# Kernel tuning notes

Measured on AMD Instinct MI355X. Metric: run time of the kernel, lower is better.

Reference implementation:

```python
import jax, jax.numpy as jnp
import numpy as np

B, T, N = 32, 24, 512
DIM_IN, DIM_OUT, HID, EMB = 64, 2, 128, 16
NEG_SLOPE = 0.01  # nn.LeakyReLU default


def leaky_relu(x):
    return jnp.where(x >= 0, x, NEG_SLOPE * x)


def setup_inputs() -> dict:
    key = jax.random.key(0)
    ks = jax.random.split(key, 11)
    return {
        "eb": jax.random.normal(ks[0], (B, T, N, DIM_IN), jnp.float32),
        "time_eb": jax.random.normal(ks[1], (B, T, EMB), jnp.float32),
        "node_eb": jax.random.normal(ks[2], (N, EMB), jnp.float32),
        # ln1: Linear(dim_in, hidden) stored as [dim_in, hidden] (x @ W + b)
        "W1": jax.random.normal(ks[3], (DIM_IN, HID), jnp.float32) / np.sqrt(DIM_IN),
        "b1": jax.random.normal(ks[4], (HID,), jnp.float32) * 0.01,
        # ln3: Linear(hidden, dim_out)
        "W3": jax.random.normal(ks[5], (HID, DIM_OUT), jnp.float32) / np.sqrt(HID),
        "b3": jax.random.normal(ks[6], (DIM_OUT,), jnp.float32) * 0.01,
        "weights_pool_spa": jax.random.normal(ks[7], (EMB, HID, HID), jnp.float32),
        "bias_pool_spa": jax.random.normal(ks[8], (EMB, HID), jnp.float32),
        "weights_pool_tem": jax.random.normal(ks[9], (EMB, HID, HID), jnp.float32),
        "bias_pool_tem": jax.random.normal(ks[10], (EMB, HID), jnp.float32),
    }


def reference(eb, time_eb, node_eb, W1, b1, W3, b3,
              weights_pool_spa, bias_pool_spa,
              weights_pool_tem, bias_pool_tem):
    # eb: [b,t,n,dim_in] -> [b,t,n,hidden]
    eb_out = eb @ W1 + b1
    # spatial hypernetwork: per-node weight [n,hid,hid] and bias [n,hid]
    weights_spa = jnp.einsum('nd,dio->nio', node_eb, weights_pool_spa)
    bias_spa = node_eb @ bias_pool_spa  # [n,hid]
    out_spa = leaky_relu(jnp.einsum('btni,nio->btno', eb_out, weights_spa) + bias_spa)
    # temporal hypernetwork: per-(b,t) weight [b,t,hid,hid] and bias [b,t,1,hid]
    weights_tem = jnp.einsum('btd,dio->btio', time_eb, weights_pool_tem)
    bias_tem = (time_eb @ bias_pool_tem)[:, :, None, :]
    out_tem = leaky_relu(jnp.einsum('btni,btio->btno', out_spa, weights_tem) + bias_tem)
    logits = out_tem @ W3 + b3  # [b,t,n,dim_out]
    return logits
```

## Files before the change

kernel.cpp:

```cpp
#include <hip/hip_runtime.h>
#include <hip/hip_bf16.h>
#include <stdint.h>

#define BT   768
#define NN   512
#define DIN  64
#define HID  128
#define EMB  16
#define SLOPE 0.01f

typedef __attribute__((ext_vector_type(8))) short bf16x8;
typedef __attribute__((ext_vector_type(4))) float f32x4;
typedef __attribute__((ext_vector_type(4))) short short4v;

__device__ __forceinline__ short f2bf(float f) {
    uint32_t u = __float_as_uint(f);
    u += 0x7fff + ((u >> 16) & 1);
    return (short)(u >> 16);
}
__device__ __forceinline__ float bf2f(short s) {
    return __uint_as_float(((uint32_t)(unsigned short)s) << 16);
}

static const size_t OFF_WCOMB = 0;
static const size_t OFF_WTEM  = 8388608;
static const size_t OFF_BSPA  = 33554432;
static const size_t OFF_BTEM  = 33816576;
static const size_t OFF_Q     = 34209792;
static const size_t OFF_PTT   = 34217984;
static const size_t OFF_PTS2  = 34742272;
static const size_t OFF_H2    = 35004416;

__global__ __launch_bounds__(256)
void k_prep(const float* __restrict__ pool_spa, const float* __restrict__ pool_tem,
            const float* __restrict__ W1, const float* __restrict__ b1,
            const float* __restrict__ bp_spa, const float* __restrict__ bp_tem,
            const float* __restrict__ node_eb, const float* __restrict__ time_eb,
            short* __restrict__ ptt, short* __restrict__ pts2,
            float* __restrict__ qtab, float* __restrict__ bspa,
            float* __restrict__ btem)
{
    const int b = blockIdx.x, t = threadIdx.x;
    __shared__ short smem[26112];

    if (b < 64) {
        const int d = b >> 2, o0 = (b & 3) * 32;
        short* s = smem;
        #pragma unroll
        for (int c = 0; c < 16; ++c) {
            int e = c * 256 + t;
            int i = e >> 5, oo = e & 31;
            s[oo * 136 + i] = f2bf(pool_tem[(d * HID + i) * HID + o0 + oo]);
        }
        __syncthreads();
        #pragma unroll
        for (int c = 0; c < 8; ++c) {
            int e = c * 256 + t;
            int oo = e >> 6, ii = (e & 63) * 2;
            uint32_t lo = (unsigned short)s[oo * 136 + ii];
            uint32_t hi = (unsigned short)s[oo * 136 + ii + 1];
            ((uint32_t*)ptt)[((d * HID + o0 + oo) * HID + ii) >> 1] = lo | (hi << 16);
        }
        return;
    }
    if (b < 224) {
        int q = (b - 64) * 256 + t;
        const float *bp, *emb; float* outp;
        if (q < NN * 32) { bp = bp_spa; emb = node_eb; outp = bspa; }
        else { q -= NN * 32; bp = bp_tem; emb = time_eb; outp = btem; }
        const int n = q >> 5, oq = q & 31;
        float4 a = make_float4(0.f, 0.f, 0.f, 0.f);
        #pragma unroll
        for (int d = 0; d < EMB; ++d) {
            float e = emb[n * EMB + d];
            float4 bv = ((const float4*)bp)[d * 32 + oq];
            a.x += e * bv.x; a.y += e * bv.y; a.z += e * bv.z; a.w += e * bv.w;
        }
        ((float4*)outp)[q] = a;
        return;
    }
    if (b < 226) {
        const int dbase = (b - 224) * 8;
        if (t < 128) {
            float a[8] = {};
            for (int i = 0; i < HID; ++i) {
                float bv = b1[i];
                #pragma unroll
                for (int dd = 0; dd < 8; ++dd)
                    a[dd] += bv * pool_spa[((dbase + dd) * HID + i) * HID + t];
            }
            #pragma unroll
            for (int dd = 0; dd < 8; ++dd) qtab[(dbase + dd) * HID + t] = a[dd];
        }
        return;
    }
    {
        const int d = b - 226;
        const int wave = t >> 6, lane = t & 63, quad = lane >> 4, l15 = lane & 15;
        const int m0 = wave * 32;
        short* sPT  = smem;
        short* sW1b = smem + 128 * 136;
        #pragma unroll
        for (int c = 0; c < 64; ++c) {
            int idx = c * 256 + t;
            int i = idx >> 7, o = idx & 127;
            sPT[o * 136 + i] = f2bf(pool_spa[(d * HID + i) * HID + o]);
        }
        #pragma unroll
        for (int c = 0; c < 32; ++c) {
            int idx = c * 256 + t;
            sW1b[(idx >> 7) * 136 + (idx & 127)] = f2bf(W1[idx]);
        }
        __syncthreads();
        f32x4 acc[2][4] = {};
        #pragma unroll
        for (int kc = 0; kc < 4; ++kc) {
            bf16x8 a0 = *(const bf16x8*)(sPT + (m0 + l15) * 136 + kc * 32 + quad * 8);
            bf16x8 a1 = *(const bf16x8*)(sPT + (m0 + 16 + l15) * 136 + kc * 32 + quad * 8);
            #pragma unroll
            for (int tc = 0; tc < 4; ++tc) {
                bf16x8 bb = *(const bf16x8*)(sW1b + (tc * 16 + l15) * 136 + kc * 32 + quad * 8);
                acc[0][tc] = __builtin_amdgcn_mfma_f32_16x16x32_bf16(a0, bb, acc[0][tc], 0, 0, 0);
                acc[1][tc] = __builtin_amdgcn_mfma_f32_16x16x32_bf16(a1, bb, acc[1][tc], 0, 0, 0);
            }
        }
        __syncthreads();
        short* sO = smem;
        #pragma unroll
        for (int tr = 0; tr < 2; ++tr)
            #pragma unroll
            for (int tc = 0; tc < 4; ++tc)
                #pragma unroll
                for (int r = 0; r < 4; ++r)
                    sO[(m0 + tr * 16 + quad * 4 + r) * 72 + tc * 16 + l15] = f2bf(acc[tr][tc][r]);
        __syncthreads();
        #pragma unroll
        for (int c = 0; c < 4; ++c) {
            int idx = c * 256 + t;
            int row = idx >> 3, ko = (idx & 7) * 8;
            *(bf16x8*)(pts2 + (size_t)d * 8192 + row * 64 + ko) =
                *(const bf16x8*)(sO + row * 72 + ko);
        }
    }
}

__global__ __launch_bounds__(256)
void k_genw(const short* __restrict__ pts2, const short* __restrict__ ptt,
            const float* __restrict__ node_eb, const float* __restrict__ time_eb,
            short* __restrict__ wcomb, short* __restrict__ wtem)
{
    const int t = threadIdx.x, b = blockIdx.x;
    int nb, cq, stride;
    const short* pool; const float* emb; short* outp;
    if (b < 64) {
        nb = b >> 3; cq = (b & 7) * 256 + t; stride = 2048;
        pool = pts2; emb = node_eb; outp = wcomb;
    } else {
        int bb = b - 64;
        nb = bb >> 4; cq = (bb & 15) * 256 + t; stride = 4096;
        pool = ptt; emb = time_eb; outp = wtem;
    }
    __shared__ float sEmb[64 * EMB];
    #pragma unroll
    for (int c = 0; c < 4; ++c) {
        int idx = c * 256 + t;
        sEmb[idx] = emb[nb * 64 * EMB + idx];
    }
    __syncthreads();
    float4 p[EMB];
    #pragma unroll
    for (int d = 0; d < EMB; ++d) {
        short4v v = ((const short4v*)pool)[d * stride + cq];
        p[d] = make_float4(bf2f(v.x), bf2f(v.y), bf2f(v.z), bf2f(v.w));
    }
    for (int nn = 0; nn < 64; ++nn) {
        float4 a = make_float4(0.f, 0.f, 0.f, 0.f);
        #pragma unroll
        for (int d = 0; d < EMB; ++d) {
            float e = sEmb[nn * EMB + d];
            a.x += e * p[d].x; a.y += e * p[d].y;
            a.z += e * p[d].z; a.w += e * p[d].w;
        }
        short4v o;
        o.x = f2bf(a.x); o.y = f2bf(a.y); o.z = f2bf(a.z); o.w = f2bf(a.w);
        ((short4v*)outp)[(size_t)(nb * 64 + nn) * stride + cq] = o;
    }
}

__global__ __launch_bounds__(256)
void k_spatial(const float* __restrict__ eb, const short* __restrict__ wcomb,
               const float* __restrict__ bspa, const float* __restrict__ qtab,
               const float* __restrict__ node_eb, short* __restrict__ h2)
{
    const int n = blockIdx.x, R0 = blockIdx.y * 64;
    const int t = threadIdx.x;
    const int wave = t >> 6, lane = t & 63, quad = lane >> 4, l15 = lane & 15;
    const int m0 = (wave >> 1) * 32, n0 = (wave & 1) * 64;

    __shared__ short smem[13824];
    short* sEb  = smem;
    short* sW   = smem + 64 * 72;
    short* sOut = smem;

    float4 ev[4];
    #pragma unroll
    for (int c = 0; c < 4; ++c) {
        int idx = c * 256 + t;
        int r = idx >> 4, kq = (idx & 15) * 4;
        ev[c] = *(const float4*)(eb + ((size_t)(R0 + r) * NN + n) * DIN + kq);
    }
    bf16x8 wreg[4];
    {
        const bf16x8* src = (const bf16x8*)(wcomb + (size_t)n * 8192);
        #pragma unroll
        for (int c = 0; c < 4; ++c) wreg[c] = src[c * 256 + t];
    }
    float bsr[4];
    #pragma unroll
    for (int tc = 0; tc < 4; ++tc) {
        int col = n0 + tc * 16 + l15;
        float a = bspa[n * HID + col];
        #pragma unroll
        for (int d = 0; d < EMB; ++d)
            a += node_eb[n * EMB + d] * qtab[d * HID + col];
        bsr[tc] = a;
    }
    #pragma unroll
    for (int c = 0; c < 4; ++c) {
        int idx = c * 256 + t;
        int r = idx >> 4, kq = (idx & 15) * 4;
        short4v s;
        s.x = f2bf(ev[c].x); s.y = f2bf(ev[c].y);
        s.z = f2bf(ev[c].z); s.w = f2bf(ev[c].w);
        *(short4v*)(sEb + r * 72 + kq) = s;
    }
    #pragma unroll
    for (int c = 0; c < 4; ++c) {
        int idx = c * 256 + t;
        *(bf16x8*)(sW + (idx >> 3) * 72 + (idx & 7) * 8) = wreg[c];
    }
    __syncthreads();

    f32x4 acc[2][4] = {};
    #pragma unroll
    for (int kc = 0; kc < 2; ++kc) {
        bf16x8 a0 = *(const bf16x8*)(sEb + (m0 + l15) * 72 + kc * 32 + quad * 8);
        bf16x8 a1 = *(const bf16x8*)(sEb + (m0 + 16 + l15) * 72 + kc * 32 + quad * 8);
        #pragma unroll
        for (int tc = 0; tc < 4; ++tc) {
            bf16x8 bfr = *(const bf16x8*)(sW + (n0 + tc * 16 + l15) * 72 + kc * 32 + quad * 8);
            acc[0][tc] = __builtin_amdgcn_mfma_f32_16x16x32_bf16(a0, bfr, acc[0][tc], 0, 0, 0);
            acc[1][tc] = __builtin_amdgcn_mfma_f32_16x16x32_bf16(a1, bfr, acc[1][tc], 0, 0, 0);
        }
    }
    __syncthreads();

    #pragma unroll
    for (int tr = 0; tr < 2; ++tr)
        #pragma unroll
        for (int tc = 0; tc < 4; ++tc) {
            int col = n0 + tc * 16 + l15;
            #pragma unroll
            for (int r = 0; r < 4; ++r) {
                float v = acc[tr][tc][r] + bsr[tc];
                v = (v >= 0.f) ? v : SLOPE * v;
                sOut[(m0 + tr * 16 + quad * 4 + r) * 136 + col] = f2bf(v);
            }
        }
    __syncthreads();
    #pragma unroll
    for (int c = 0; c < 4; ++c) {
        int idx = c * 256 + t;
        int row = idx >> 4, col = (idx & 15) * 8;
        *(bf16x8*)(h2 + ((size_t)(R0 + row) * NN + n) * HID + col) =
            *(const bf16x8*)(sOut + row * 136 + col);
    }
}

__global__ __launch_bounds__(256)
void k_temporal(const short* __restrict__ h2, const short* __restrict__ wtem,
                const float* __restrict__ btem, const float* __restrict__ W3,
                const float* __restrict__ b3, float* __restrict__ out)
{
    const int R = blockIdx.x, nbase = blockIdx.y * 256;
    const int t = threadIdx.x;
    const int wave = t >> 6, lane = t & 63, quad = lane >> 4, l15 = lane & 15;
    const int m0 = wave * 16;

    __shared__ short sWt[128 * 136];
    __shared__ short sH2[64 * 136];

    bf16x8 wv[8];
    {
        const bf16x8* src = (const bf16x8*)(wtem + (size_t)R * 16384);
        #pragma unroll
        for (int c = 0; c < 8; ++c) wv[c] = src[c * 256 + t];
    }
    bf16x8 hreg[4];
    {
        const bf16x8* src = (const bf16x8*)(h2 + ((size_t)R * NN + nbase) * HID);
        #pragma unroll
        for (int c = 0; c < 4; ++c) hreg[c] = src[c * 256 + t];
    }
    float btr[8], w3r0[8], w3r1[8];
    #pragma unroll
    for (int tc = 0; tc < 8; ++tc) {
        int o = tc * 16 + l15;
        btr[tc] = btem[R * HID + o];
        w3r0[tc] = W3[2 * o]; w3r1[tc] = W3[2 * o + 1];
    }
    const float b30 = b3[0], b31 = b3[1];

    #pragma unroll
    for (int c = 0; c < 8; ++c) {
        int idx = c * 256 + t;
        *(bf16x8*)(sWt + (idx >> 4) * 136 + (idx & 15) * 8) = wv[c];
    }
    #pragma unroll
    for (int c = 0; c < 4; ++c) {
        int idx = c * 256 + t;
        *(bf16x8*)(sH2 + (idx >> 4) * 136 + (idx & 15) * 8) = hreg[c];
    }
    __syncthreads();

    for (int nt = 0; nt < 4; ++nt) {
        if (nt < 3) {
            const bf16x8* src = (const bf16x8*)(h2 + ((size_t)R * NN + nbase + (nt + 1) * 64) * HID);
            #pragma unroll
            for (int c = 0; c < 4; ++c) hreg[c] = src[c * 256 + t];
        }
        f32x4 acc[8] = {};
        #pragma unroll
        for (int kc = 0; kc < 4; ++kc) {
            bf16x8 a = *(const bf16x8*)(sH2 + (m0 + l15) * 136 + kc * 32 + quad * 8);
            #pragma unroll
            for (int tc = 0; tc < 8; ++tc) {
                bf16x8 b = *(const bf16x8*)(sWt + (tc * 16 + l15) * 136 + kc * 32 + quad * 8);
                acc[tc] = __builtin_amdgcn_mfma_f32_16x16x32_bf16(a, b, acc[tc], 0, 0, 0);
            }
        }
        float pl[4][2] = {};
        #pragma unroll
        for (int tc = 0; tc < 8; ++tc) {
            #pragma unroll
            for (int r = 0; r < 4; ++r) {
                float v = acc[tc][r] + btr[tc];
                v = (v >= 0.f) ? v : SLOPE * v;
                pl[r][0] += v * w3r0[tc];
                pl[r][1] += v * w3r1[tc];
            }
        }
        #pragma unroll
        for (int m = 1; m <= 8; m <<= 1)
            #pragma unroll
            for (int r = 0; r < 4; ++r) {
                pl[r][0] += __shfl_xor(pl[r][0], m);
                pl[r][1] += __shfl_xor(pl[r][1], m);
            }
        if (l15 == 0) {
            #pragma unroll
            for (int r = 0; r < 4; ++r) {
                int nrow = nbase + nt * 64 + m0 + quad * 4 + r;
                *(float2*)(out + ((size_t)R * NN + nrow) * 2) =
                    make_float2(pl[r][0] + b30, pl[r][1] + b31);
            }
        }
        __syncthreads();
        if (nt < 3) {
            #pragma unroll
            for (int c = 0; c < 4; ++c) {
                int idx = c * 256 + t;
                *(bf16x8*)(sH2 + (idx >> 4) * 136 + (idx & 15) * 8) = hreg[c];
            }
            __syncthreads();
        }
    }
}

extern "C" void kernel_launch(void* const* d_in, const int* in_sizes, int n_in,
                              void* d_out, int out_size, void* d_ws, size_t ws_size,
                              hipStream_t stream) {
    const float* eb        = (const float*)d_in[0];
    const float* time_eb   = (const float*)d_in[1];
    const float* node_eb   = (const float*)d_in[2];
    const float* W1        = (const float*)d_in[3];
    const float* b1        = (const float*)d_in[4];
    const float* W3        = (const float*)d_in[5];
    const float* b3        = (const float*)d_in[6];
    const float* pool_spa  = (const float*)d_in[7];
    const float* bpool_spa = (const float*)d_in[8];
    const float* pool_tem  = (const float*)d_in[9];
    const float* bpool_tem = (const float*)d_in[10];
    float* out = (float*)d_out;

    char* ws = (char*)d_ws;
    short* wcomb = (short*)(ws + OFF_WCOMB);
    short* wtem  = (short*)(ws + OFF_WTEM);
    float* bspa  = (float*)(ws + OFF_BSPA);
    float* btem  = (float*)(ws + OFF_BTEM);
    float* qtab  = (float*)(ws + OFF_Q);
    short* ptt   = (short*)(ws + OFF_PTT);
    short* pts2  = (short*)(ws + OFF_PTS2);
    short* h2    = (short*)(ws + OFF_H2);

    k_prep<<<242, 256, 0, stream>>>(pool_spa, pool_tem, W1, b1, bpool_spa, bpool_tem,
                                    node_eb, time_eb, ptt, pts2, qtab, bspa, btem);
    k_genw<<<256, 256, 0, stream>>>(pts2, ptt, node_eb, time_eb, wcomb, wtem);
    k_spatial<<<dim3(NN, 12), 256, 0, stream>>>(eb, wcomb, bspa, qtab, node_eb, h2);
    k_temporal<<<dim3(BT, 2), 256, 0, stream>>>(h2, wtem, btem, W3, b3, out);
}
```

Baseline: 257.0 us.

## Make spatial kernel persistent per node with double-buffered eb prefetch

The spatial kernel now launches one block per node instead of 12 blocks per node. Each block loads the node's combined weight and bias once, then loops over 12 row chunks. The next chunk's eb rows are prefetched into registers and written into a second shared buffer while the current chunk runs on MFMA. This removes 11 of every 12 redundant weight loads and bias computations and overlaps global loads with compute. In exchange the grid shrinks from 6144 to 512 blocks, which may underfill the GPU's compute units and lengthen each block's serial chain.

```diff
diff --git a/kernel.cpp b/kernel.cpp
--- a/kernel.cpp
+++ b/kernel.cpp
@@ -192,29 +192,31 @@
                const float* __restrict__ bspa, const float* __restrict__ qtab,
                const float* __restrict__ node_eb, short* __restrict__ h2)
 {
-    const int n = blockIdx.x, R0 = blockIdx.y * 64;
+    const int n = blockIdx.x;
     const int t = threadIdx.x;
     const int wave = t >> 6, lane = t & 63, quad = lane >> 4, l15 = lane & 15;
     const int m0 = (wave >> 1) * 32, n0 = (wave & 1) * 64;
 
-    __shared__ short smem[13824];
-    short* sEb  = smem;
-    short* sW   = smem + 64 * 72;
-    short* sOut = smem;
-
-    float4 ev[4];
-    #pragma unroll
-    for (int c = 0; c < 4; ++c) {
-        int idx = c * 256 + t;
-        int r = idx >> 4, kq = (idx & 15) * 4;
-        ev[c] = *(const float4*)(eb + ((size_t)(R0 + r) * NN + n) * DIN + kq);
-    }
+    __shared__ short sW[128 * 72];
+    __shared__ short sEb[2][64 * 72];
+    __shared__ short sOut[64 * 136];
+
+    const float* ebn = eb + (size_t)n * DIN;
+    short* h2n = h2 + (size_t)n * HID;
+
     bf16x8 wreg[4];
     {
         const bf16x8* src = (const bf16x8*)(wcomb + (size_t)n * 8192);
         #pragma unroll
         for (int c = 0; c < 4; ++c) wreg[c] = src[c * 256 + t];
     }
+    float4 ev[4];
+    #pragma unroll
+    for (int c = 0; c < 4; ++c) {
+        int idx = c * 256 + t;
+        int r = idx >> 4, kq = (idx & 15) * 4;
+        ev[c] = *(const float4*)(ebn + (size_t)r * (NN * DIN) + kq);
+    }
     float bsr[4];
     #pragma unroll
     for (int tc = 0; tc < 4; ++tc) {
@@ -224,6 +226,11 @@
         for (int d = 0; d < EMB; ++d)
             a += node_eb[n * EMB + d] * qtab[d * HID + col];
         bsr[tc] = a;
+    }
+    #pragma unroll
+    for (int c = 0; c < 4; ++c) {
+        int idx = c * 256 + t;
+        *(bf16x8*)(sW + (idx >> 3) * 72 + (idx & 7) * 8) = wreg[c];
     }
     #pragma unroll
     for (int c = 0; c < 4; ++c) {
@@ -232,48 +239,64 @@
         short4v s;
         s.x = f2bf(ev[c].x); s.y = f2bf(ev[c].y);
         s.z = f2bf(ev[c].z); s.w = f2bf(ev[c].w);
-        *(short4v*)(sEb + r * 72 + kq) = s;
-    }
-    #pragma unroll
-    for (int c = 0; c < 4; ++c) {
-        int idx = c * 256 + t;
-        *(bf16x8*)(sW + (idx >> 3) * 72 + (idx & 7) * 8) = wreg[c];
+        *(short4v*)(sEb[0] + r * 72 + kq) = s;
     }
     __syncthreads();
 
-    f32x4 acc[2][4] = {};
-    #pragma unroll
-    for (int kc = 0; kc < 2; ++kc) {
-        bf16x8 a0 = *(const bf16x8*)(sEb + (m0 + l15) * 72 + kc * 32 + quad * 8);
-        bf16x8 a1 = *(const bf16x8*)(sEb + (m0 + 16 + l15) * 72 + kc * 32 + quad * 8);
-        #pragma unroll
-        for (int tc = 0; tc < 4; ++tc) {
-            bf16x8 bfr = *(const bf16x8*)(sW + (n0 + tc * 16 + l15) * 72 + kc * 32 + quad * 8);
-            acc[0][tc] = __builtin_amdgcn_mfma_f32_16x16x32_bf16(a0, bfr, acc[0][tc], 0, 0, 0);
-            acc[1][tc] = __builtin_amdgcn_mfma_f32_16x16x32_bf16(a1, bfr, acc[1][tc], 0, 0, 0);
-        }
-    }
-    __syncthreads();
-
-    #pragma unroll
-    for (int tr = 0; tr < 2; ++tr)
-        #pragma unroll
-        for (int tc = 0; tc < 4; ++tc) {
-            int col = n0 + tc * 16 + l15;
-            #pragma unroll
-            for (int r = 0; r < 4; ++r) {
-                float v = acc[tr][tc][r] + bsr[tc];
-                v = (v >= 0.f) ? v : SLOPE * v;
-                sOut[(m0 + tr * 16 + quad * 4 + r) * 136 + col] = f2bf(v);
-            }
-        }
-    __syncthreads();
-    #pragma unroll
-    for (int c = 0; c < 4; ++c) {
-        int idx = c * 256 + t;
-        int row = idx >> 4, col = (idx & 15) * 8;
-        *(bf16x8*)(h2 + ((size_t)(R0 + row) * NN + n) * HID + col) =
-            *(const bf16x8*)(sOut + row * 136 + col);
+    for (int ch = 0; ch < 12; ++ch) {
+        const int cur = ch & 1, nxt = cur ^ 1;
+        if (ch < 11) {
+            #pragma unroll
+            for (int c = 0; c < 4; ++c) {
+                int idx = c * 256 + t;
+                int r = (ch + 1) * 64 + (idx >> 4), kq = (idx & 15) * 4;
+                ev[c] = *(const float4*)(ebn + (size_t)r * (NN * DIN) + kq);
+            }
+        }
+        f32x4 acc[2][4] = {};
+        #pragma unroll
+        for (int kc = 0; kc < 2; ++kc) {
+            bf16x8 a0 = *(const bf16x8*)(sEb[cur] + (m0 + l15) * 72 + kc * 32 + quad * 8);
+            bf16x8 a1 = *(const bf16x8*)(sEb[cur] + (m0 + 16 + l15) * 72 + kc * 32 + quad * 8);
+            #pragma unroll
+            for (int tc = 0; tc < 4; ++tc) {
+                bf16x8 bfr = *(const bf16x8*)(sW + (n0 + tc * 16 + l15) * 72 + kc * 32 + quad * 8);
+                acc[0][tc] = __builtin_amdgcn_mfma_f32_16x16x32_bf16(a0, bfr, acc[0][tc], 0, 0, 0);
+                acc[1][tc] = __builtin_amdgcn_mfma_f32_16x16x32_bf16(a1, bfr, acc[1][tc], 0, 0, 0);
+            }
+        }
+        #pragma unroll
+        for (int tr = 0; tr < 2; ++tr)
+            #pragma unroll
+            for (int tc = 0; tc < 4; ++tc) {
+                int col = n0 + tc * 16 + l15;
+                #pragma unroll
+                for (int r = 0; r < 4; ++r) {
+                    float v = acc[tr][tc][r] + bsr[tc];
+                    v = (v >= 0.f) ? v : SLOPE * v;
+                    sOut[(m0 + tr * 16 + quad * 4 + r) * 136 + col] = f2bf(v);
+                }
+            }
+        if (ch < 11) {
+            #pragma unroll
+            for (int c = 0; c < 4; ++c) {
+                int idx = c * 256 + t;
+                int r = idx >> 4, kq = (idx & 15) * 4;
+                short4v s;
+                s.x = f2bf(ev[c].x); s.y = f2bf(ev[c].y);
+                s.z = f2bf(ev[c].z); s.w = f2bf(ev[c].w);
+                *(short4v*)(sEb[nxt] + r * 72 + kq) = s;
+            }
+        }
+        __syncthreads();
+        #pragma unroll
+        for (int c = 0; c < 4; ++c) {
+            int idx = c * 256 + t;
+            int row = idx >> 4, col = (idx & 15) * 8;
+            *(bf16x8*)(h2n + (size_t)(ch * 64 + row) * (NN * HID) + col) =
+                *(const bf16x8*)(sOut + row * 136 + col);
+        }
+        __syncthreads();
     }
 }
 
@@ -406,6 +429,6 @@
     k_prep<<<242, 256, 0, stream>>>(pool_spa, pool_tem, W1, b1, bpool_spa, bpool_tem,
                                     node_eb, time_eb, ptt, pts2, qtab, bspa, btem);
     k_genw<<<256, 256, 0, stream>>>(pts2, ptt, node_eb, time_eb, wcomb, wtem);
-    k_spatial<<<dim3(NN, 12), 256, 0, stream>>>(eb, wcomb, bspa, qtab, node_eb, h2);
+    k_spatial<<<dim3(NN), 256, 0, stream>>>(eb, wcomb, bspa, qtab, node_eb, h2);
     k_temporal<<<dim3(BT, 2), 256, 0, stream>>>(h2, wtem, btem, W3, b3, out);
 }
```

New measurement: 251.5 us. 2.1% less time.
